# Kernel optimization log

Hardware: AMD Instinct MI355X
Metric: run time of the kernel (lower is better)

## Reference

```python
import jax, jax.numpy as jnp
import numpy as np

HEAD_DIM = 128
N_Q_HEADS = 16
N_KV_HEADS = 8
ROPE_THETA = 10000.0


def setup_inputs() -> dict:
    key = jax.random.key(0)
    ks = jax.random.split(key, 5)
    B, S, D, Hq, Hkv = 2, 2048, 4096, 2048, 1024
    sc = 0.02
    hidden_states = jax.random.normal(ks[0], (B, S, D), dtype=jnp.float32)
    wq = jax.random.normal(ks[1], (Hq, D), dtype=jnp.float32) * sc
    wk = jax.random.normal(ks[2], (Hkv, D), dtype=jnp.float32) * sc
    wv = jax.random.normal(ks[3], (Hkv, D), dtype=jnp.float32) * sc
    wo = jax.random.normal(ks[4], (D, Hq), dtype=jnp.float32) * sc
    position_ids = jnp.broadcast_to(jnp.arange(S, dtype=jnp.int64)[None, :], (B, S))
    return {"hidden_states": hidden_states, "position_ids": position_ids,
            "wq": wq, "wk": wk, "wv": wv, "wo": wo}


def _rope_cos_sin(position_ids, dtype):
    # Llama rotary embedding: inv_freq over even dims, emb = cat(freqs, freqs)
    inv_freq = 1.0 / (ROPE_THETA ** (jnp.arange(0, HEAD_DIM, 2, dtype=jnp.float32) / HEAD_DIM))
    freqs = position_ids.astype(jnp.float32)[:, :, None] * inv_freq[None, None, :]  # [B,S,d/2]
    emb = jnp.concatenate([freqs, freqs], axis=-1)  # [B,S,d]
    return jnp.cos(emb).astype(dtype), jnp.sin(emb).astype(dtype)


def _rotate_half(x):
    x1, x2 = jnp.split(x, 2, axis=-1)
    return jnp.concatenate([-x2, x1], axis=-1)


def reference(hidden_states, position_ids, wq, wk, wv, wo):
    B, S, D = hidden_states.shape
    dh = HEAD_DIM
    q = (hidden_states @ wq.T).reshape(B, S, N_Q_HEADS, dh).transpose(0, 2, 1, 3)   # [B,Hq,S,d]
    k = (hidden_states @ wk.T).reshape(B, S, N_KV_HEADS, dh).transpose(0, 2, 1, 3)  # [B,Hkv,S,d]
    v = (hidden_states @ wv.T).reshape(B, S, N_KV_HEADS, dh).transpose(0, 2, 1, 3)

    cos, sin = _rope_cos_sin(position_ids, q.dtype)  # [B,S,d]
    cos, sin = cos[:, None, :, :], sin[:, None, :, :]
    q = q * cos + _rotate_half(q) * sin
    k = k * cos + _rotate_half(k) * sin

    # GQA repeat_interleave(groups, dim=1)
    groups = N_Q_HEADS // N_KV_HEADS
    k = jnp.repeat(k, groups, axis=1)  # [B,Hq,S,d]
    v = jnp.repeat(v, groups, axis=1)

    scale = 1.0 / jnp.sqrt(jnp.asarray(dh, dtype=q.dtype))
    scores = jnp.einsum('bhqd,bhkd->bhqk', q, k) * scale
    causal = jnp.tril(jnp.ones((S, S), dtype=bool))
    scores = jnp.where(causal[None, None, :, :], scores, jnp.finfo(scores.dtype).min)
    probs = jax.nn.softmax(scores, axis=-1)
    attn = jnp.einsum('bhqk,bhkd->bhqd', probs, v)  # [B,Hq,S,d]
    attn = attn.transpose(0, 2, 1, 3).reshape(B, S, N_Q_HEADS * dh)
    return attn @ wo.T
```

## Files before the change

### kernel.cpp

```cpp
#include <hip/hip_runtime.h>
#include <cstdint>
#include <cstddef>

#define B_ 2
#define S_ 2048
#define NQKV 4096
#define HQ 16
#define HKV 8
#define DH 128
#define KOFF 2048
#define VOFF 3072

typedef __attribute__((ext_vector_type(4))) float f32x4;
typedef __attribute__((ext_vector_type(8))) short bf16x8;
typedef __attribute__((ext_vector_type(4))) unsigned int u32x4;
typedef const __attribute__((address_space(1))) void* gas1;
typedef __attribute__((address_space(3))) void* las3;
typedef __attribute__((address_space(3))) char* l3p;

__device__ __forceinline__ ushort f2b(float f) {
  union { float f; unsigned u; } x; x.f = f;
  return (ushort)((x.u + 0x7FFFu + ((x.u >> 16) & 1u)) >> 16);
}
__device__ __forceinline__ float b2f(ushort u) {
  union { unsigned u; float f; } x; x.u = ((unsigned)u) << 16; return x.f;
}

__global__ void cast_f32_bf16_kernel(const float4* __restrict__ in, ushort4* __restrict__ out) {
  int i = blockIdx.x * 256 + threadIdx.x;
  float4 v = in[i];
  out[i] = make_ushort4(f2b(v.x), f2b(v.y), f2b(v.z), f2b(v.w));
}

__global__ void cast_wcat_kernel(const float* __restrict__ wq, const float* __restrict__ wk,
                                 const float* __restrict__ wv, ushort4* __restrict__ out) {
  int i = blockIdx.x * 256 + threadIdx.x;
  int row = i >> 10, c4 = i & 1023;
  const float* src = (row < 2048) ? (wq + (size_t)row * 4096)
                   : (row < 3072) ? (wk + (size_t)(row - 2048) * 4096)
                                  : (wv + (size_t)(row - 3072) * 4096);
  float4 v = ((const float4*)src)[c4];
  out[i] = make_ushort4(f2b(v.x), f2b(v.y), f2b(v.z), f2b(v.w));
}

#define DSR(dst, addr, off) asm volatile("ds_read_b128 %0, %1 offset:" #off : "=v"(dst) : "v"(addr) : "memory")
#define MFMA16(d, a, b) d = __builtin_amdgcn_mfma_f32_16x16x32_bf16(a, b, d, 0, 0, 0)

template<int OUT_BF16>
__launch_bounds__(512, 2)
__global__ void gemm256(const ushort* __restrict__ A, const ushort* __restrict__ Bm,
                        void* __restrict__ C, int M, int N, int K) {
  __shared__ __attribute__((aligned(16))) char lds[131072];
  const int tid = threadIdx.x;
  const int lane = tid & 63;
  const int w = tid >> 6;
  const int wm = w >> 2, wn = w & 3;
  const int lr = lane & 15, lg = lane >> 4;

  const int nwg = gridDim.x;
  const int cpx = nwg >> 3;
  const int wg = blockIdx.x;
  const int swz = (wg & 7) * cpx + (wg >> 3);
  const int NT = N >> 8;
  const int bm = swz / NT, bn = swz % NT;
  const int m0 = bm * 256, n0 = bn * 256;

  const ushort* Ab = A + (size_t)m0 * K;
  const ushort* Bb = Bm + (size_t)n0 * K;

  const int NKT = K >> 6;

  int srow[2], scol[2];
#pragma unroll
  for (int jj = 0; jj < 2; ++jj) {
    int lb = (jj * 512 + tid) * 16;
    int ls = lb ^ (((lb >> 7) & 7) << 4);
    srow[jj] = ls >> 7;
    scol[jj] = (ls & 127) >> 1;
  }
  const int ldsw = w * 1024;

  auto stage2 = [&](int t, int j) {
    t = (t < NKT - 1) ? t : (NKT - 1);
    const int slot = ((t & 1) << 16) + (j << 14);
    const ushort* src = (j == 1 || j == 2) ? Ab : Bb;
    const int h = (j >= 2) ? 128 : 0;
    const int k0 = t << 6;
#pragma unroll
    for (int jj = 0; jj < 2; ++jj) {
      const ushort* g = src + (size_t)(h + srow[jj]) * K + k0 + scol[jj];
      __builtin_amdgcn_global_load_lds((gas1)(const void*)g,
          (las3)(void*)(lds + slot + jj * 8192 + ldsw), 16, 0, 0);
    }
  };

  const unsigned lds0 = (unsigned)(size_t)(l3p)(void*)lds;
  const int swzc = (lr & 7) << 4;
  const int c0 = (lg * 16) ^ swzc;
  const int c1 = (64 + lg * 16) ^ swzc;
  const unsigned baseA = lds0 + 16384u + wm * 16384u + lr * 128u;
  const unsigned baseB = lds0 + ((wn >> 1) ? 49152u : 0u) + ((wn & 1) * 64 + lr) * 128u;

  f32x4 zero = {0.0f, 0.0f, 0.0f, 0.0f};
  f32x4 acc[8][4];
#pragma unroll
  for (int m = 0; m < 8; ++m)
#pragma unroll
    for (int n = 0; n < 4; ++n) acc[m][n] = zero;

  stage2(0, 0); stage2(0, 1); stage2(0, 2); stage2(0, 3);
  stage2(1, 0); stage2(1, 1);
  asm volatile("s_waitcnt vmcnt(4)" ::: "memory");
  __builtin_amdgcn_s_barrier();

  for (int kt = 0; kt < NKT; ++kt) {
    const unsigned bo = (unsigned)((kt & 1) << 16);
    const unsigned aak0 = baseA + c0 + bo, aak1 = baseA + c1 + bo;
    const unsigned bak0 = baseB + c0 + bo, bak1 = baseB + c1 + bo;

    bf16x8 a0[2][4], a1[2][4], bq[2][2], bq2[2][2];

    DSR(a0[0][0], aak0, 0);    DSR(a0[0][1], aak0, 2048);
    DSR(a0[0][2], aak0, 4096); DSR(a0[0][3], aak0, 6144);
    DSR(a0[1][0], aak1, 0);    DSR(a0[1][1], aak1, 2048);
    DSR(a0[1][2], aak1, 4096); DSR(a0[1][3], aak1, 6144);
    DSR(bq[0][0], bak0, 0);    DSR(bq[0][1], bak0, 2048);
    DSR(bq[1][0], bak1, 0);    DSR(bq[1][1], bak1, 2048);
    stage2(kt + 1, 2);
    asm volatile("s_waitcnt lgkmcnt(8)" ::: "memory");
    __builtin_amdgcn_s_barrier();
    asm volatile("s_waitcnt lgkmcnt(0)" ::: "memory");
    __builtin_amdgcn_sched_barrier(0);
    __builtin_amdgcn_s_setprio(1);
#pragma unroll
    for (int kk = 0; kk < 2; ++kk)
#pragma unroll
      for (int m = 0; m < 4; ++m) {
        MFMA16(acc[m][0], a0[kk][m], bq[kk][0]);
        MFMA16(acc[m][1], a0[kk][m], bq[kk][1]);
      }
    __builtin_amdgcn_s_setprio(0);
    __builtin_amdgcn_s_barrier();

    DSR(bq2[0][0], bak0, 4096); DSR(bq2[0][1], bak0, 6144);
    DSR(bq2[1][0], bak1, 4096); DSR(bq2[1][1], bak1, 6144);
    stage2(kt + 1, 3);
    __builtin_amdgcn_s_barrier();
    asm volatile("s_waitcnt lgkmcnt(0)" ::: "memory");
    __builtin_amdgcn_sched_barrier(0);
    __builtin_amdgcn_s_setprio(1);
#pragma unroll
    for (int kk = 0; kk < 2; ++kk)
#pragma unroll
      for (int m = 0; m < 4; ++m) {
        MFMA16(acc[m][2], a0[kk][m], bq2[kk][0]);
        MFMA16(acc[m][3], a0[kk][m], bq2[kk][1]);
      }
    __builtin_amdgcn_s_setprio(0);
    __builtin_amdgcn_s_barrier();

    DSR(a1[0][0], aak0, 8192);  DSR(a1[0][1], aak0, 10240);
    DSR(a1[0][2], aak0, 12288); DSR(a1[0][3], aak0, 14336);
    DSR(a1[1][0], aak1, 8192);  DSR(a1[1][1], aak1, 10240);
    DSR(a1[1][2], aak1, 12288); DSR(a1[1][3], aak1, 14336);
    stage2(kt + 2, 0);
    __builtin_amdgcn_s_barrier();
    asm volatile("s_waitcnt lgkmcnt(0)" ::: "memory");
    __builtin_amdgcn_sched_barrier(0);
    __builtin_amdgcn_s_setprio(1);
#pragma unroll
    for (int kk = 0; kk < 2; ++kk)
#pragma unroll
      for (int m = 0; m < 4; ++m) {
        MFMA16(acc[m + 4][0], a1[kk][m], bq[kk][0]);
        MFMA16(acc[m + 4][1], a1[kk][m], bq[kk][1]);
      }
    __builtin_amdgcn_s_setprio(0);
    __builtin_amdgcn_s_barrier();

    stage2(kt + 2, 1);
    __builtin_amdgcn_s_barrier();
    __builtin_amdgcn_s_setprio(1);
#pragma unroll
    for (int kk = 0; kk < 2; ++kk)
#pragma unroll
      for (int m = 0; m < 4; ++m) {
        MFMA16(acc[m + 4][2], a1[kk][m], bq2[kk][0]);
        MFMA16(acc[m + 4][3], a1[kk][m], bq2[kk][1]);
      }
    __builtin_amdgcn_s_setprio(0);
    asm volatile("s_waitcnt vmcnt(4)" ::: "memory");
    __builtin_amdgcn_s_barrier();
  }

  asm volatile("s_waitcnt vmcnt(0)" ::: "memory");

#pragma unroll
  for (int m = 0; m < 8; ++m) {
    const int row0 = m0 + wm * 128 + m * 16 + lg * 4;
#pragma unroll
    for (int n = 0; n < 4; ++n) {
      const int col = n0 + wn * 64 + n * 16 + lr;
#pragma unroll
      for (int r = 0; r < 4; ++r) {
        if (OUT_BF16) ((ushort*)C)[(size_t)(row0 + r) * N + col] = f2b(acc[m][n][r]);
        else          ((float*)C)[(size_t)(row0 + r) * N + col] = acc[m][n][r];
      }
    }
  }
}

__global__ void rope_kernel(ushort* __restrict__ qkv) {
  int t = blockIdx.x * 256 + threadIdx.x;
  int row = t / 1536;
  int idx = t - row * 1536;
  int head = idx >> 6, d = idx & 63;
  int pos = row & (S_ - 1);
  int col = (head < HQ) ? (head * DH + d) : (KOFF + (head - HQ) * DH + d);
  size_t base = (size_t)row * NQKV + col;
  float x1 = b2f(qkv[base]);
  float x2 = b2f(qkv[base + 64]);
  float inv = exp2f((float)d * -0.2076205059304600f);
  float ang = (float)pos * inv;
  float c = cosf(ang), s = sinf(ang);
  qkv[base]      = f2b(x1 * c - x2 * s);
  qkv[base + 64] = f2b(x2 * c + x1 * s);
}

__global__ void transpose_v_kernel(const ushort* __restrict__ qkv, ushort* __restrict__ vt) {
  __shared__ ushort tile[32][33];
  const int s0 = blockIdx.x * 32, d0 = blockIdx.y * 32;
  const int bh = blockIdx.z, b = bh >> 3, kvh = bh & 7;
  const int tx = threadIdx.x, ty = threadIdx.y;
  const ushort* src = qkv + (size_t)(b * S_ + s0) * NQKV + VOFF + kvh * DH + d0;
#pragma unroll
  for (int j = 0; j < 32; j += 8)
    tile[ty + j][tx] = src[(size_t)(ty + j) * NQKV + tx];
  __syncthreads();
  ushort* dst = vt + (size_t)((b * HKV + kvh) * DH + d0) * S_ + s0;
#pragma unroll
  for (int j = 0; j < 32; j += 8)
    dst[(size_t)(ty + j) * S_ + tx] = tile[tx][ty + j];
}

__launch_bounds__(256, 2)
__global__ void attn_kernel(const ushort* __restrict__ qkv, const ushort* __restrict__ vt,
                            ushort* __restrict__ aout) {
  __shared__ ushort Ks[64 * DH];
  __shared__ ushort Vts[DH * 64];
  __shared__ ushort Ps[4][16 * 64];
  const int tid = threadIdx.x, lane = tid & 63, w = tid >> 6;
  const int wg = blockIdx.x;
  const int swz = (wg & 7) * 64 + (wg >> 3);
  const int bh = swz >> 4, qi0 = swz & 15;
  const int b = bh >> 4, h = bh & 15, kvh = h >> 1;
  const int lr = lane & 15, lg = lane >> 4;

  const ushort* Kp = qkv + (size_t)(b * S_) * NQKV + KOFF + kvh * DH;
  const ushort* Vtp = vt + (size_t)(b * HKV + kvh) * DH * S_;
  ushort* Psw = &Ps[w][0];

  int koff[4], kb[4], voff[4], vb[4];
#pragma unroll
  for (int i = 0; i < 4; ++i) {
    int chunk = i * 256 + tid;
    int krow = chunk >> 4, kc = (chunk & 15) * 8;
    koff[i] = krow * NQKV + kc;
    kb[i] = (krow * 256 + kc * 2) ^ ((krow & 7) << 4);
    int vrow = chunk >> 3, vc = (chunk & 7) * 8;
    voff[i] = vrow * S_ + vc;
    vb[i] = (vrow * 128 + vc * 2) ^ ((vrow & 7) << 4);
  }

  f32x4 zero = {0.0f, 0.0f, 0.0f, 0.0f};
  const float SCALE_LOG2E = 0.12751744116470802f;

  for (int pass = 0; pass < 2; ++pass) {
    const int qi = pass ? (31 - qi0) : qi0;
    const int qt0 = qi * 64;
    const int qrow = qt0 + w * 16;

    bf16x8 qf[4];
    {
      const ushort* Qp = qkv + (size_t)(b * S_ + qrow + lr) * NQKV + h * DH;
#pragma unroll
      for (int ds = 0; ds < 4; ++ds)
        qf[ds] = *(const bf16x8*)(Qp + ds * 32 + lg * 8);
    }

    float m_run[4], l_run[4];
    f32x4 acc_o[8];
#pragma unroll
    for (int r = 0; r < 4; ++r) { m_run[r] = -1e30f; l_run[r] = 0.0f; }
#pragma unroll
    for (int n = 0; n < 8; ++n) acc_o[n] = zero;

    const int ntiles = qi + 1;
    u32x4 kreg[4], vreg[4];

#pragma unroll
    for (int i = 0; i < 4; ++i) {
      kreg[i] = *(const u32x4*)(Kp + koff[i]);
      vreg[i] = *(const u32x4*)(Vtp + voff[i]);
    }
    __syncthreads();
#pragma unroll
    for (int i = 0; i < 4; ++i) {
      *(u32x4*)((char*)Ks + kb[i]) = kreg[i];
      *(u32x4*)((char*)Vts + vb[i]) = vreg[i];
    }
    __syncthreads();

    for (int t = 0; t < ntiles; ++t) {
      const int kv0 = t * 64;
      if (t + 1 < ntiles) {
        const int kv1 = kv0 + 64;
#pragma unroll
        for (int i = 0; i < 4; ++i) {
          kreg[i] = *(const u32x4*)(Kp + (size_t)kv1 * NQKV + koff[i]);
          vreg[i] = *(const u32x4*)(Vtp + kv1 + voff[i]);
        }
      }

      f32x4 sacc[4];
#pragma unroll
      for (int ct = 0; ct < 4; ++ct) {
        sacc[ct] = zero;
#pragma unroll
        for (int ds = 0; ds < 4; ++ds) {
          int krow = ct * 16 + lr;
          int kbb = (krow * 256 + (ds * 32 + lg * 8) * 2) ^ ((krow & 7) << 4);
          bf16x8 kf = *(const bf16x8*)((const char*)Ks + kbb);
          sacc[ct] = __builtin_amdgcn_mfma_f32_16x16x32_bf16(qf[ds], kf, sacc[ct], 0, 0, 0);
        }
      }

#pragma unroll
      for (int r = 0; r < 4; ++r) {
        const int q = qrow + lg * 4 + r;
        float sv[4];
#pragma unroll
        for (int ct = 0; ct < 4; ++ct) {
          int kv = kv0 + ct * 16 + lr;
          float x = sacc[ct][r] * SCALE_LOG2E;
          sv[ct] = (kv <= q) ? x : -1e30f;
        }
        float mx = fmaxf(fmaxf(sv[0], sv[1]), fmaxf(sv[2], sv[3]));
#pragma unroll
        for (int o = 1; o < 16; o <<= 1) mx = fmaxf(mx, __shfl_xor(mx, o, 64));
        if (!__all(mx <= m_run[r] + 8.0f)) {
          float mnew = fmaxf(m_run[r], mx);
          float alpha = __builtin_amdgcn_exp2f(m_run[r] - mnew);
          l_run[r] *= alpha;
#pragma unroll
          for (int n = 0; n < 8; ++n) acc_o[n][r] *= alpha;
          m_run[r] = mnew;
        }
        float psum = 0.0f;
#pragma unroll
        for (int ct = 0; ct < 4; ++ct) {
          float p = __builtin_amdgcn_exp2f(sv[ct] - m_run[r]);
          psum += p;
          int prow = lg * 4 + r;
          int pb = (prow * 128 + (ct * 16 + lr) * 2) ^ ((prow & 7) << 4);
          *(ushort*)((char*)Psw + pb) = f2b(p);
        }
#pragma unroll
        for (int o = 1; o < 16; o <<= 1) psum += __shfl_xor(psum, o, 64);
        l_run[r] += psum;
      }

      asm volatile("s_waitcnt lgkmcnt(0)" ::: "memory");
      __builtin_amdgcn_sched_barrier(0);

#pragma unroll
      for (int ks = 0; ks < 2; ++ks) {
        int pb = (lr * 128 + (ks * 32 + lg * 8) * 2) ^ ((lr & 7) << 4);
        bf16x8 pf = *(const bf16x8*)((const char*)Psw + pb);
#pragma unroll
        for (int n = 0; n < 8; ++n) {
          int vrow = n * 16 + lr;
          int vbb = (vrow * 128 + (ks * 32 + lg * 8) * 2) ^ ((vrow & 7) << 4);
          bf16x8 vf = *(const bf16x8*)((const char*)Vts + vbb);
          acc_o[n] = __builtin_amdgcn_mfma_f32_16x16x32_bf16(pf, vf, acc_o[n], 0, 0, 0);
        }
      }

      if (t + 1 < ntiles) {
        __syncthreads();
#pragma unroll
        for (int i = 0; i < 4; ++i) {
          *(u32x4*)((char*)Ks + kb[i]) = kreg[i];
          *(u32x4*)((char*)Vts + vb[i]) = vreg[i];
        }
        __syncthreads();
      }
    }

    float rl[4];
#pragma unroll
    for (int r = 0; r < 4; ++r) rl[r] = 1.0f / l_run[r];
    ushort* Ap = aout + (size_t)(b * S_ + qrow) * 2048 + h * DH;
#pragma unroll
    for (int n = 0; n < 8; ++n) {
#pragma unroll
      for (int r = 0; r < 4; ++r) {
        float val = acc_o[n][r] * rl[r];
        Ap[(size_t)(lg * 4 + r) * 2048 + n * 16 + lr] = f2b(val);
      }
    }
  }
}

extern "C" void kernel_launch(void* const* d_in, const int* in_sizes, int n_in,
                              void* d_out, int out_size, void* d_ws, size_t ws_size,
                              hipStream_t stream) {
  const float* hs = (const float*)d_in[0];
  const float* wq = (const float*)d_in[2];
  const float* wk = (const float*)d_in[3];
  const float* wv = (const float*)d_in[4];
  const float* wo = (const float*)d_in[5];
  char* ws = (char*)d_ws;

  ushort* Xb   = (ushort*)(ws + 0);
  ushort* Wcat = (ushort*)(ws + 33554432);
  ushort* QKV  = (ushort*)(ws + 67108864);
  ushort* Vt   = (ushort*)(ws + 100663296);
  ushort* Wob  = Xb;
  ushort* Aout = Wcat;

  cast_f32_bf16_kernel<<<16384, 256, 0, stream>>>((const float4*)hs, (ushort4*)Xb);
  cast_wcat_kernel<<<16384, 256, 0, stream>>>(wq, wk, wv, (ushort4*)Wcat);
  gemm256<1><<<256, 512, 0, stream>>>(Xb, Wcat, QKV, 4096, 4096, 4096);
  rope_kernel<<<24576, 256, 0, stream>>>(QKV);
  transpose_v_kernel<<<dim3(64, 4, 16), dim3(32, 8), 0, stream>>>(QKV, Vt);
  cast_f32_bf16_kernel<<<8192, 256, 0, stream>>>((const float4*)wo, (ushort4*)Wob);
  attn_kernel<<<dim3(512), 256, 0, stream>>>(QKV, Vt, Aout);
  gemm256<0><<<256, 512, 0, stream>>>(Aout, Wob, (float*)d_out, 4096, 4096, 2048);
}
```

Before: 363.2 us.

## Transpose attention MFMA operands so each lane owns one query row

Swaps the A/B operands of both MFMAs so the score and output accumulators hold transposed results, with each lane owning a single query row. This lets the softmax keep one running max and sum per lane, reduced with two cross-lane shuffles instead of four-step reductions repeated for four rows. The output is staged through a new per-wave LDS buffer and written as 16-byte coalesced stores rather than scattered 2-byte stores. s_setprio is raised around the MFMA sections. The change adds 16 KB of LDS per block, which may affect the occupancy of two blocks per CU.

After: 312.8 us. 1.16x faster.

```diff
diff --git a/kernel.cpp b/kernel.cpp
--- a/kernel.cpp
+++ b/kernel.cpp
@@ -249,6 +249,7 @@
   __shared__ ushort Ks[64 * DH];
   __shared__ ushort Vts[DH * 64];
   __shared__ ushort Ps[4][16 * 64];
+  __shared__ ushort Es[4][16 * 128];
   const int tid = threadIdx.x, lane = tid & 63, w = tid >> 6;
   const int wg = blockIdx.x;
   const int swz = (wg & 7) * 64 + (wg >> 3);
@@ -279,6 +280,7 @@
     const int qi = pass ? (31 - qi0) : qi0;
     const int qt0 = qi * 64;
     const int qrow = qt0 + w * 16;
+    const int q_lane = qrow + lr;
 
     bf16x8 qf[4];
     {
@@ -288,10 +290,8 @@
         qf[ds] = *(const bf16x8*)(Qp + ds * 32 + lg * 8);
     }
 
-    float m_run[4], l_run[4];
+    float m_run = -1e30f, l_run = 0.0f;
     f32x4 acc_o[8];
-#pragma unroll
-    for (int r = 0; r < 4; ++r) { m_run[r] = -1e30f; l_run[r] = 0.0f; }
 #pragma unroll
     for (int n = 0; n < 8; ++n) acc_o[n] = zero;
 
@@ -323,6 +323,7 @@
       }
 
       f32x4 sacc[4];
+      __builtin_amdgcn_s_setprio(1);
 #pragma unroll
       for (int ct = 0; ct < 4; ++ct) {
         sacc[ct] = zero;
@@ -331,48 +332,53 @@
           int krow = ct * 16 + lr;
           int kbb = (krow * 256 + (ds * 32 + lg * 8) * 2) ^ ((krow & 7) << 4);
           bf16x8 kf = *(const bf16x8*)((const char*)Ks + kbb);
-          sacc[ct] = __builtin_amdgcn_mfma_f32_16x16x32_bf16(qf[ds], kf, sacc[ct], 0, 0, 0);
-        }
-      }
-
-#pragma unroll
-      for (int r = 0; r < 4; ++r) {
-        const int q = qrow + lg * 4 + r;
-        float sv[4];
-#pragma unroll
-        for (int ct = 0; ct < 4; ++ct) {
-          int kv = kv0 + ct * 16 + lr;
+          sacc[ct] = __builtin_amdgcn_mfma_f32_16x16x32_bf16(kf, qf[ds], sacc[ct], 0, 0, 0);
+        }
+      }
+      __builtin_amdgcn_s_setprio(0);
+
+      float sv[4][4];
+      float mx = -1e30f;
+#pragma unroll
+      for (int ct = 0; ct < 4; ++ct)
+#pragma unroll
+        for (int r = 0; r < 4; ++r) {
+          int kv = kv0 + ct * 16 + lg * 4 + r;
           float x = sacc[ct][r] * SCALE_LOG2E;
-          sv[ct] = (kv <= q) ? x : -1e30f;
-        }
-        float mx = fmaxf(fmaxf(sv[0], sv[1]), fmaxf(sv[2], sv[3]));
-#pragma unroll
-        for (int o = 1; o < 16; o <<= 1) mx = fmaxf(mx, __shfl_xor(mx, o, 64));
-        if (!__all(mx <= m_run[r] + 8.0f)) {
-          float mnew = fmaxf(m_run[r], mx);
-          float alpha = __builtin_amdgcn_exp2f(m_run[r] - mnew);
-          l_run[r] *= alpha;
-#pragma unroll
-          for (int n = 0; n < 8; ++n) acc_o[n][r] *= alpha;
-          m_run[r] = mnew;
-        }
-        float psum = 0.0f;
-#pragma unroll
-        for (int ct = 0; ct < 4; ++ct) {
-          float p = __builtin_amdgcn_exp2f(sv[ct] - m_run[r]);
+          sv[ct][r] = (kv <= q_lane) ? x : -1e30f;
+          mx = fmaxf(mx, sv[ct][r]);
+        }
+      mx = fmaxf(mx, __shfl_xor(mx, 16, 64));
+      mx = fmaxf(mx, __shfl_xor(mx, 32, 64));
+      if (!__all(mx <= m_run + 8.0f)) {
+        float mnew = fmaxf(m_run, mx);
+        float alpha = __builtin_amdgcn_exp2f(m_run - mnew);
+        l_run *= alpha;
+#pragma unroll
+        for (int n = 0; n < 8; ++n)
+#pragma unroll
+          for (int r = 0; r < 4; ++r) acc_o[n][r] *= alpha;
+        m_run = mnew;
+      }
+      float psum = 0.0f;
+#pragma unroll
+      for (int ct = 0; ct < 4; ++ct)
+#pragma unroll
+        for (int r = 0; r < 4; ++r) {
+          float p = __builtin_amdgcn_exp2f(sv[ct][r] - m_run);
           psum += p;
-          int prow = lg * 4 + r;
-          int pb = (prow * 128 + (ct * 16 + lr) * 2) ^ ((prow & 7) << 4);
+          int kvl = ct * 16 + lg * 4 + r;
+          int pb = (lr * 128 + kvl * 2) ^ ((lr & 7) << 4);
           *(ushort*)((char*)Psw + pb) = f2b(p);
         }
-#pragma unroll
-        for (int o = 1; o < 16; o <<= 1) psum += __shfl_xor(psum, o, 64);
-        l_run[r] += psum;
-      }
+      psum += __shfl_xor(psum, 16, 64);
+      psum += __shfl_xor(psum, 32, 64);
+      l_run += psum;
 
       asm volatile("s_waitcnt lgkmcnt(0)" ::: "memory");
       __builtin_amdgcn_sched_barrier(0);
 
+      __builtin_amdgcn_s_setprio(1);
 #pragma unroll
       for (int ks = 0; ks < 2; ++ks) {
         int pb = (lr * 128 + (ks * 32 + lg * 8) * 2) ^ ((lr & 7) << 4);
@@ -382,9 +388,10 @@
           int vrow = n * 16 + lr;
           int vbb = (vrow * 128 + (ks * 32 + lg * 8) * 2) ^ ((vrow & 7) << 4);
           bf16x8 vf = *(const bf16x8*)((const char*)Vts + vbb);
-          acc_o[n] = __builtin_amdgcn_mfma_f32_16x16x32_bf16(pf, vf, acc_o[n], 0, 0, 0);
-        }
-      }
+          acc_o[n] = __builtin_amdgcn_mfma_f32_16x16x32_bf16(vf, pf, acc_o[n], 0, 0, 0);
+        }
+      }
+      __builtin_amdgcn_s_setprio(0);
 
       if (t + 1 < ntiles) {
         __syncthreads();
@@ -397,17 +404,26 @@
       }
     }
 
-    float rl[4];
-#pragma unroll
-    for (int r = 0; r < 4; ++r) rl[r] = 1.0f / l_run[r];
+    float rl = 1.0f / l_run;
+    char* Ew = (char*)&Es[w][0];
+#pragma unroll
+    for (int n = 0; n < 8; ++n)
+#pragma unroll
+      for (int rp = 0; rp < 2; ++rp) {
+        unsigned lo = f2b(acc_o[n][2 * rp] * rl);
+        unsigned hi = f2b(acc_o[n][2 * rp + 1] * rl);
+        int d = n * 16 + lg * 4 + 2 * rp;
+        int eb = (lr * 256 + d * 2) ^ ((lr & 7) << 4);
+        *(unsigned*)(Ew + eb) = lo | (hi << 16);
+      }
     ushort* Ap = aout + (size_t)(b * S_ + qrow) * 2048 + h * DH;
 #pragma unroll
-    for (int n = 0; n < 8; ++n) {
-#pragma unroll
-      for (int r = 0; r < 4; ++r) {
-        float val = acc_o[n][r] * rl[r];
-        Ap[(size_t)(lg * 4 + r) * 2048 + n * 16 + lr] = f2b(val);
-      }
+    for (int it = 0; it < 4; ++it) {
+      int c = it * 64 + lane;
+      int q = c >> 4, k16 = c & 15;
+      int rb = (q * 256 + k16 * 16) ^ ((q & 7) << 4);
+      u32x4 v = *(const u32x4*)(Ew + rb);
+      *(u32x4*)((char*)(Ap + (size_t)q * 2048) + k16 * 16) = v;
     }
   }
 }
```
